# Kernel tuning notes

Hardware: AMD Instinct MI355X
Metric: run time of the kernel (lower is better)

The kernel has to match this reference:

```python
import jax, jax.numpy as jnp
import numpy as np

NEG_INF = -1e9  # matches masked_fill value -1000000000.0
SLOPE = 0.2     # LeakyReLU negative slope


def setup_inputs() -> dict:
    key = jax.random.key(0)
    k1, k2, k3, k4 = jax.random.split(key, 4)
    B, N, Fin, Fout = 16, 1024, 256, 256
    h = jax.random.normal(k1, (B, N, Fin), dtype=jnp.float32)
    adj = jax.random.randint(k2, (B, N, N), 0, 2, dtype=jnp.int32)
    W = jax.random.normal(k3, (Fin, Fout), dtype=jnp.float32) * (1.0 / np.sqrt(Fin))
    a = jax.random.normal(k4, (2 * Fout,), dtype=jnp.float32) * (1.0 / np.sqrt(2 * Fout))
    return {"h": h, "adj": adj, "W": W, "a": a}


def reference(h, adj, W, a):
    # h: [B,N,Fin], adj: [B,N,N] (0/1), W: [Fin,Fout], a: [2*Fout]
    Fout = W.shape[1]
    Wh = jnp.einsum("bnf,fo->bno", h, W)            # [B,N,Fout]
    a1, a2 = a[:Fout], a[Fout:]
    # e[b,i,j] = leakyrelu( Wh[b,i]·a1 + Wh[b,j]·a2 )  == a(cat(Wh_i, Wh_j))
    f1 = Wh @ a1                                     # [B,N]
    f2 = Wh @ a2                                     # [B,N]
    e = jax.nn.leaky_relu(f1[:, :, None] + f2[:, None, :], negative_slope=SLOPE)
    e = jnp.where(adj == 0, NEG_INF, e)              # mask non-edges
    attention = jax.nn.softmax(e, axis=-1)           # [B,N,N]
    # dropout is identity at eval / p=0
    h_prime = jnp.einsum("bij,bjo->bio", attention, Wh)  # [B,N,Fout]
    return h_prime
```

## Files before the change

kernel.cpp:

```cpp
#include <hip/hip_runtime.h>

typedef __attribute__((ext_vector_type(8))) short bf16x8;
typedef __attribute__((ext_vector_type(4))) float f32x4;

__device__ __forceinline__ unsigned short f2bf(float x) {
    unsigned int u = __float_as_uint(x);
    u += 0x7FFFu + ((u >> 16) & 1u);
    return (unsigned short)(u >> 16);
}

__global__ __launch_bounds__(256) void prep(const float* __restrict__ W,
                                            short* __restrict__ WbT) {
    __shared__ float tile[32][33];
    const int t = threadIdx.x;
    const int bx = blockIdx.x & 7, by = blockIdx.x >> 3;
    const int r0 = by * 32, c0 = bx * 32;
    const int lr = t >> 5, lc = t & 31;
#pragma unroll
    for (int q = 0; q < 4; ++q)
        tile[q * 8 + lr][lc] = W[(r0 + q * 8 + lr) * 256 + c0 + lc];
    __syncthreads();
#pragma unroll
    for (int q = 0; q < 4; ++q)
        WbT[(c0 + q * 8 + lr) * 256 + r0 + lc] = (short)f2bf(tile[lc][q * 8 + lr]);
}

__global__ __launch_bounds__(256, 4) void wh_f12(const float* __restrict__ h,
                                                 const short* __restrict__ WbT,
                                                 const float* __restrict__ a,
                                                 short* __restrict__ WhT,
                                                 float* __restrict__ f1,
                                                 float* __restrict__ f2) {
    __shared__ short hA[32][264];
    __shared__ float sp[2][4][32];
    const int t = threadIdx.x;
    const int wid = t >> 6, lane = t & 63;
    const int quad = lane >> 4, l15 = lane & 15;
    const int m0 = blockIdx.x * 32;

#pragma unroll
    for (int rr = 0; rr < 2; ++rr) {
        const int r = rr * 16 + (t >> 4), c0 = (t & 15) * 16;
        const float* hp = h + (size_t)(m0 + r) * 256 + c0;
        float4 v0 = *(const float4*)(hp + 0), v1 = *(const float4*)(hp + 4);
        float4 v2 = *(const float4*)(hp + 8), v3 = *(const float4*)(hp + 12);
        bf16x8 w0, w1;
        w0[0] = (short)f2bf(v0.x); w0[1] = (short)f2bf(v0.y);
        w0[2] = (short)f2bf(v0.z); w0[3] = (short)f2bf(v0.w);
        w0[4] = (short)f2bf(v1.x); w0[5] = (short)f2bf(v1.y);
        w0[6] = (short)f2bf(v1.z); w0[7] = (short)f2bf(v1.w);
        w1[0] = (short)f2bf(v2.x); w1[1] = (short)f2bf(v2.y);
        w1[2] = (short)f2bf(v2.z); w1[3] = (short)f2bf(v2.w);
        w1[4] = (short)f2bf(v3.x); w1[5] = (short)f2bf(v3.y);
        w1[6] = (short)f2bf(v3.z); w1[7] = (short)f2bf(v3.w);
        *(bf16x8*)&hA[r][c0] = w0;
        *(bf16x8*)&hA[r][c0 + 8] = w1;
    }
    __syncthreads();

    f32x4 acc[2][4] = {};
#pragma unroll
    for (int kt = 0; kt < 8; ++kt) {
        const int k0 = kt * 32;
        bf16x8 bv[4];
#pragma unroll
        for (int ft = 0; ft < 4; ++ft)
            bv[ft] = *(const bf16x8*)(WbT + (size_t)(wid * 64 + ft * 16 + l15) * 256 + k0 + quad * 8);
        bf16x8 a0 = *(const bf16x8*)&hA[l15][k0 + quad * 8];
        bf16x8 a1 = *(const bf16x8*)&hA[16 + l15][k0 + quad * 8];
#pragma unroll
        for (int ft = 0; ft < 4; ++ft) {
            acc[0][ft] = __builtin_amdgcn_mfma_f32_16x16x32_bf16(a0, bv[ft], acc[0][ft], 0, 0, 0);
            acc[1][ft] = __builtin_amdgcn_mfma_f32_16x16x32_bf16(a1, bv[ft], acc[1][ft], 0, 0, 0);
        }
    }

    const int b = m0 >> 10;
#pragma unroll
    for (int mf = 0; mf < 2; ++mf) {
        const int il0 = (m0 & 1023) + mf * 16 + quad * 4;
#pragma unroll
        for (int ft = 0; ft < 4; ++ft) {
            const int f = wid * 64 + ft * 16 + l15;
            ushort4 pk;
            pk.x = f2bf(acc[mf][ft][0]);
            pk.y = f2bf(acc[mf][ft][1]);
            pk.z = f2bf(acc[mf][ft][2]);
            pk.w = f2bf(acc[mf][ft][3]);
            *(ushort4*)(WhT + ((size_t)b << 18) + (size_t)f * 1024 + il0) = pk;
        }
    }

    float a1v[4], a2v[4];
#pragma unroll
    for (int ft = 0; ft < 4; ++ft) {
        a1v[ft] = a[wid * 64 + ft * 16 + l15];
        a2v[ft] = a[256 + wid * 64 + ft * 16 + l15];
    }
    float p1[2][4] = {}, p2[2][4] = {};
#pragma unroll
    for (int mf = 0; mf < 2; ++mf)
#pragma unroll
        for (int ft = 0; ft < 4; ++ft)
#pragma unroll
            for (int r = 0; r < 4; ++r) {
                p1[mf][r] += acc[mf][ft][r] * a1v[ft];
                p2[mf][r] += acc[mf][ft][r] * a2v[ft];
            }
#pragma unroll
    for (int off = 1; off < 16; off <<= 1)
#pragma unroll
        for (int mf = 0; mf < 2; ++mf)
#pragma unroll
            for (int r = 0; r < 4; ++r) {
                p1[mf][r] += __shfl_xor(p1[mf][r], off);
                p2[mf][r] += __shfl_xor(p2[mf][r], off);
            }
    if (l15 == 0)
#pragma unroll
        for (int mf = 0; mf < 2; ++mf)
#pragma unroll
            for (int r = 0; r < 4; ++r) {
                sp[0][wid][mf * 16 + quad * 4 + r] = p1[mf][r];
                sp[1][wid][mf * 16 + quad * 4 + r] = p2[mf][r];
            }
    __syncthreads();
    if (t < 32) {
        f1[m0 + t] = sp[0][0][t] + sp[0][1][t] + sp[0][2][t] + sp[0][3][t];
        f2[m0 + t] = sp[1][0][t] + sp[1][1][t] + sp[1][2][t] + sp[1][3][t];
    }
}

__global__ __launch_bounds__(512, 2) void fused_agg(const int* __restrict__ adj,
                                                    const float* __restrict__ f1g,
                                                    const float* __restrict__ f2g,
                                                    const short* __restrict__ WhT,
                                                    float* __restrict__ out) {
    __shared__ short Ps[64 * 1024];
    __shared__ float lred[512];
    __shared__ float linv[64];

    const int t = threadIdx.x;
    const int wid = t >> 6, lane = t & 63;
    const int quad = lane >> 4, l15 = lane & 15;

    const int id = blockIdx.x;
    const int xcd = id & 7, rest = id >> 3;
    const int b = xcd + 8 * (rest & 1);
    const int m0 = (rest >> 1) * 64;

    const int r = t >> 3, jc = t & 7;
    const float f1r = f1g[(b << 10) + m0 + r];
    const int* arow = adj + ((size_t)b << 20) + (size_t)(m0 + r) * 1024 + jc * 8;
    const float* f2p = f2g + (b << 10) + jc * 8;
    short* prow = Ps + r * 1024;
    const int rx = r & 7;
    float lacc = 0.f;
#pragma unroll 4
    for (int i = 0; i < 16; ++i) {
        int4 a0 = *(const int4*)(arow + i * 64);
        int4 a1 = *(const int4*)(arow + i * 64 + 4);
        float4 w0 = *(const float4*)(f2p + i * 64);
        float4 w1 = *(const float4*)(f2p + i * 64 + 4);
        float xs[8] = {w0.x, w0.y, w0.z, w0.w, w1.x, w1.y, w1.z, w1.w};
        int ms[8] = {a0.x, a0.y, a0.z, a0.w, a1.x, a1.y, a1.z, a1.w};
        bf16x8 pw;
#pragma unroll
        for (int u = 0; u < 8; ++u) {
            float x = f1r + xs[u];
            x = fmaxf(x, 0.2f * x);
            float pv = ms[u] ? __expf(x) : 0.f;
            lacc += pv;
            pw[u] = (short)f2bf(pv);
        }
        *(bf16x8*)(prow + (((i * 8 + jc) ^ rx) * 8)) = pw;
    }
    lred[t] = lacc;
    __syncthreads();

    const int wm = wid >> 2, wn = wid & 3;
    const int mh = wm * 32, nq = wn * 64;
    const short* Wb = WhT + ((size_t)b << 18);
    const short* pB0 = Wb + (size_t)(nq + l15) * 1024 + quad * 8;
    const short* pB1 = pB0 + 16 * 1024;
    const short* pB2 = pB0 + 32 * 1024;
    const short* pB3 = pB0 + 48 * 1024;
    const short* rowA0 = Ps + (size_t)(mh + l15) * 1024;
    const short* rowA1 = rowA0 + 16 * 1024;
    const int sx = l15 & 7;

    f32x4 acc[2][4] = {};
    bf16x8 bA[8], bB[8];

    auto loadB = [&](bf16x8* dst, int T) {
#pragma unroll
        for (int kt = 0; kt < 2; ++kt) {
            dst[kt * 4 + 0] = *(const bf16x8*)(pB0 + T * 64 + kt * 32);
            dst[kt * 4 + 1] = *(const bf16x8*)(pB1 + T * 64 + kt * 32);
            dst[kt * 4 + 2] = *(const bf16x8*)(pB2 + T * 64 + kt * 32);
            dst[kt * 4 + 3] = *(const bf16x8*)(pB3 + T * 64 + kt * 32);
        }
    };
    auto tile = [&](bf16x8* bv, int T) {
#pragma unroll
        for (int kt = 0; kt < 2; ++kt) {
            const int sw = ((T * 8 + kt * 4 + quad) ^ sx) * 8;
            bf16x8 av0 = *(const bf16x8*)(rowA0 + sw);
            bf16x8 av1 = *(const bf16x8*)(rowA1 + sw);
#pragma unroll
            for (int nf = 0; nf < 4; ++nf) {
                acc[0][nf] = __builtin_amdgcn_mfma_f32_16x16x32_bf16(av0, bv[kt * 4 + nf], acc[0][nf], 0, 0, 0);
                acc[1][nf] = __builtin_amdgcn_mfma_f32_16x16x32_bf16(av1, bv[kt * 4 + nf], acc[1][nf], 0, 0, 0);
            }
        }
    };

    loadB(bA, 0);
#pragma unroll
    for (int tp = 0; tp < 8; ++tp) {
        const int t0 = tp * 2, t1 = t0 + 1;
        loadB(bB, t1);
        tile(bA, t0);
        if (t1 < 15) loadB(bA, t1 + 1);
        tile(bB, t1);
    }

    if (t < 64) {
        const float* lp = lred + t * 8;
        linv[t] = 1.0f / (((lp[0] + lp[1]) + (lp[2] + lp[3])) +
                          ((lp[4] + lp[5]) + (lp[6] + lp[7])));
    }
    __syncthreads();

#pragma unroll
    for (int mf = 0; mf < 2; ++mf) {
        const int il = mh + mf * 16 + quad * 4;
        const float i0 = linv[il], i1 = linv[il + 1];
        const float i2 = linv[il + 2], i3 = linv[il + 3];
#pragma unroll
        for (int nf = 0; nf < 4; ++nf) {
            float* op = out + (size_t)((b << 10) + m0 + il) * 256 + nq + nf * 16 + l15;
            op[0]   = acc[mf][nf][0] * i0;
            op[256] = acc[mf][nf][1] * i1;
            op[512] = acc[mf][nf][2] * i2;
            op[768] = acc[mf][nf][3] * i3;
        }
    }
}

extern "C" void kernel_launch(void* const* d_in, const int* in_sizes, int n_in,
                              void* d_out, int out_size, void* d_ws, size_t ws_size,
                              hipStream_t stream) {
    const float* h   = (const float*)d_in[0];
    const int*   adj = (const int*)d_in[1];
    const float* W   = (const float*)d_in[2];
    const float* a   = (const float*)d_in[3];
    float* out = (float*)d_out;

    short* WbT = (short*)d_ws;
    float* f1  = (float*)(WbT + 65536);
    float* f2  = f1 + 16384;
    short* WhT = (short*)(f2 + 16384);

    prep<<<64, 256, 0, stream>>>(W, WbT);
    wh_f12<<<512, 256, 0, stream>>>(h, WbT, a, WhT, f1, f2);
    fused_agg<<<256, 512, 0, stream>>>(adj, f1, f2, WhT, out);
}
```

Measured before the change: 154.5 us.

## Halve row tile to 32 rows, double grid and occupancy in fused aggregation

After: 152.4 us. About the same (-1.3%).

```diff
diff --git a/kernel.cpp b/kernel.cpp
--- a/kernel.cpp
+++ b/kernel.cpp
@@ -131,14 +131,14 @@
     }
 }
 
-__global__ __launch_bounds__(512, 2) void fused_agg(const int* __restrict__ adj,
+__global__ __launch_bounds__(512, 4) void fused_agg(const int* __restrict__ adj,
                                                     const float* __restrict__ f1g,
                                                     const float* __restrict__ f2g,
                                                     const short* __restrict__ WhT,
                                                     float* __restrict__ out) {
-    __shared__ short Ps[64 * 1024];
+    __shared__ short Ps[16 * 32 * 64];
     __shared__ float lred[512];
-    __shared__ float linv[64];
+    __shared__ float linv[32];
 
     const int t = threadIdx.x;
     const int wid = t >> 6, lane = t & 63;
@@ -147,71 +147,64 @@
     const int id = blockIdx.x;
     const int xcd = id & 7, rest = id >> 3;
     const int b = xcd + 8 * (rest & 1);
-    const int m0 = (rest >> 1) * 64;
-
-    const int r = t >> 3, jc = t & 7;
+    const int m0 = (rest >> 1) * 32;
+
+    const int r = t >> 4, sub = t & 15;
+    const int rx = r & 7;
     const float f1r = f1g[(b << 10) + m0 + r];
-    const int* arow = adj + ((size_t)b << 20) + (size_t)(m0 + r) * 1024 + jc * 8;
-    const float* f2p = f2g + (b << 10) + jc * 8;
-    short* prow = Ps + r * 1024;
-    const int rx = r & 7;
+    const int* arow = adj + ((size_t)b << 20) + (size_t)(m0 + r) * 1024 + sub * 4;
+    const float* f2p = f2g + (b << 10) + sub * 4;
+    short* pdst = Ps + r * 64 + ((sub >> 1) ^ rx) * 8 + (sub & 1) * 4;
     float lacc = 0.f;
 #pragma unroll 4
     for (int i = 0; i < 16; ++i) {
-        int4 a0 = *(const int4*)(arow + i * 64);
-        int4 a1 = *(const int4*)(arow + i * 64 + 4);
-        float4 w0 = *(const float4*)(f2p + i * 64);
-        float4 w1 = *(const float4*)(f2p + i * 64 + 4);
-        float xs[8] = {w0.x, w0.y, w0.z, w0.w, w1.x, w1.y, w1.z, w1.w};
-        int ms[8] = {a0.x, a0.y, a0.z, a0.w, a1.x, a1.y, a1.z, a1.w};
-        bf16x8 pw;
-#pragma unroll
-        for (int u = 0; u < 8; ++u) {
-            float x = f1r + xs[u];
-            x = fmaxf(x, 0.2f * x);
-            float pv = ms[u] ? __expf(x) : 0.f;
-            lacc += pv;
-            pw[u] = (short)f2bf(pv);
-        }
-        *(bf16x8*)(prow + (((i * 8 + jc) ^ rx) * 8)) = pw;
+        int4 av = *(const int4*)(arow + i * 64);
+        float4 fv = *(const float4*)(f2p + i * 64);
+        float x0 = f1r + fv.x, x1 = f1r + fv.y, x2 = f1r + fv.z, x3 = f1r + fv.w;
+        x0 = fmaxf(x0, 0.2f * x0);
+        x1 = fmaxf(x1, 0.2f * x1);
+        x2 = fmaxf(x2, 0.2f * x2);
+        x3 = fmaxf(x3, 0.2f * x3);
+        float p0 = av.x ? __expf(x0) : 0.f;
+        float p1 = av.y ? __expf(x1) : 0.f;
+        float p2 = av.z ? __expf(x2) : 0.f;
+        float p3 = av.w ? __expf(x3) : 0.f;
+        lacc += (p0 + p1) + (p2 + p3);
+        ushort4 pk;
+        pk.x = f2bf(p0); pk.y = f2bf(p1); pk.z = f2bf(p2); pk.w = f2bf(p3);
+        *(ushort4*)(pdst + i * 2048) = pk;
     }
     lred[t] = lacc;
     __syncthreads();
 
-    const int wm = wid >> 2, wn = wid & 3;
-    const int mh = wm * 32, nq = wn * 64;
+    const int n0 = wid * 32;
     const short* Wb = WhT + ((size_t)b << 18);
-    const short* pB0 = Wb + (size_t)(nq + l15) * 1024 + quad * 8;
+    const short* pB0 = Wb + (size_t)(n0 + l15) * 1024 + quad * 8;
     const short* pB1 = pB0 + 16 * 1024;
-    const short* pB2 = pB0 + 32 * 1024;
-    const short* pB3 = pB0 + 48 * 1024;
-    const short* rowA0 = Ps + (size_t)(mh + l15) * 1024;
-    const short* rowA1 = rowA0 + 16 * 1024;
+    const short* rowA0 = Ps + l15 * 64;
+    const short* rowA1 = Ps + (16 + l15) * 64;
     const int sx = l15 & 7;
 
-    f32x4 acc[2][4] = {};
-    bf16x8 bA[8], bB[8];
+    f32x4 acc[2][2] = {};
+    bf16x8 bA[4], bB[4];
 
     auto loadB = [&](bf16x8* dst, int T) {
 #pragma unroll
         for (int kt = 0; kt < 2; ++kt) {
-            dst[kt * 4 + 0] = *(const bf16x8*)(pB0 + T * 64 + kt * 32);
-            dst[kt * 4 + 1] = *(const bf16x8*)(pB1 + T * 64 + kt * 32);
-            dst[kt * 4 + 2] = *(const bf16x8*)(pB2 + T * 64 + kt * 32);
-            dst[kt * 4 + 3] = *(const bf16x8*)(pB3 + T * 64 + kt * 32);
+            dst[kt * 2 + 0] = *(const bf16x8*)(pB0 + T * 64 + kt * 32);
+            dst[kt * 2 + 1] = *(const bf16x8*)(pB1 + T * 64 + kt * 32);
         }
     };
-    auto tile = [&](bf16x8* bv, int T) {
+    auto tile = [&](const bf16x8* bv, int T) {
 #pragma unroll
         for (int kt = 0; kt < 2; ++kt) {
-            const int sw = ((T * 8 + kt * 4 + quad) ^ sx) * 8;
+            const int sw = T * 2048 + (((kt * 4 + quad) ^ sx) * 8);
             bf16x8 av0 = *(const bf16x8*)(rowA0 + sw);
             bf16x8 av1 = *(const bf16x8*)(rowA1 + sw);
-#pragma unroll
-            for (int nf = 0; nf < 4; ++nf) {
-                acc[0][nf] = __builtin_amdgcn_mfma_f32_16x16x32_bf16(av0, bv[kt * 4 + nf], acc[0][nf], 0, 0, 0);
-                acc[1][nf] = __builtin_amdgcn_mfma_f32_16x16x32_bf16(av1, bv[kt * 4 + nf], acc[1][nf], 0, 0, 0);
-            }
+            acc[0][0] = __builtin_amdgcn_mfma_f32_16x16x32_bf16(av0, bv[kt * 2 + 0], acc[0][0], 0, 0, 0);
+            acc[0][1] = __builtin_amdgcn_mfma_f32_16x16x32_bf16(av0, bv[kt * 2 + 1], acc[0][1], 0, 0, 0);
+            acc[1][0] = __builtin_amdgcn_mfma_f32_16x16x32_bf16(av1, bv[kt * 2 + 0], acc[1][0], 0, 0, 0);
+            acc[1][1] = __builtin_amdgcn_mfma_f32_16x16x32_bf16(av1, bv[kt * 2 + 1], acc[1][1], 0, 0, 0);
         }
     };
 
@@ -225,21 +218,23 @@
         tile(bB, t1);
     }
 
-    if (t < 64) {
-        const float* lp = lred + t * 8;
-        linv[t] = 1.0f / (((lp[0] + lp[1]) + (lp[2] + lp[3])) +
-                          ((lp[4] + lp[5]) + (lp[6] + lp[7])));
+    if (t < 32) {
+        const float* lp = lred + t * 16;
+        float s = 0.f;
+#pragma unroll
+        for (int q = 0; q < 16; ++q) s += lp[q];
+        linv[t] = 1.0f / s;
     }
     __syncthreads();
 
 #pragma unroll
     for (int mf = 0; mf < 2; ++mf) {
-        const int il = mh + mf * 16 + quad * 4;
+        const int il = mf * 16 + quad * 4;
         const float i0 = linv[il], i1 = linv[il + 1];
         const float i2 = linv[il + 2], i3 = linv[il + 3];
 #pragma unroll
-        for (int nf = 0; nf < 4; ++nf) {
-            float* op = out + (size_t)((b << 10) + m0 + il) * 256 + nq + nf * 16 + l15;
+        for (int nf = 0; nf < 2; ++nf) {
+            float* op = out + (size_t)((b << 10) + m0 + il) * 256 + n0 + nf * 16 + l15;
             op[0]   = acc[mf][nf][0] * i0;
             op[256] = acc[mf][nf][1] * i1;
             op[512] = acc[mf][nf][2] * i2;
@@ -264,5 +259,5 @@
 
     prep<<<64, 256, 0, stream>>>(W, WbT);
     wh_f12<<<512, 256, 0, stream>>>(h, WbT, a, WhT, f1, f2);
-    fused_agg<<<256, 512, 0, stream>>>(adj, f1, f2, WhT, out);
-}
+    fused_agg<<<512, 512, 0, stream>>>(adj, f1, f2, WhT, out);
+}
```
